# Optimization experiments

Hardware: AMD Instinct MI355X
Metric: run time of the kernel (lower is better)

The kernel has to match this reference:

```python
import jax, jax.numpy as jnp
import numpy as np

F = 39          # total fields = 13 numeric + 26 categorical
NUM_NUM = 13
N_CAT = 26
V = 100000      # vocab per categorical field
E = 16          # embed size
RED = max(1, F // 3)  # SE reduction size = 13
P = F * (F - 1) // 2  # 741 pairs
HID = [1024, 512, 256]
B = 4096

I_IDX, J_IDX = np.triu_indices(F, k=1)  # static pair indices, len P


def setup_inputs() -> dict:
    key = jax.random.key(0)
    ks = jax.random.split(key, 16)
    s = 0.01
    inp = {
        "cat": jax.random.randint(ks[0], (B, N_CAT), 0, V),
        "num": jax.random.normal(ks[1], (B, NUM_NUM), dtype=jnp.float32),
        "embed_tables": jax.random.normal(ks[2], (N_CAT, V, E), dtype=jnp.float32) * s,
        "num_emb": jax.random.normal(ks[3], (NUM_NUM, E), dtype=jnp.float32) * s,
        "W_se1": jax.random.normal(ks[4], (F, RED), dtype=jnp.float32) * 0.1,
        "W_se2": jax.random.normal(ks[5], (RED, F), dtype=jnp.float32) * 0.1,
        "W_bil": jax.random.normal(ks[6], (F, E, E), dtype=jnp.float32) * 0.1,  # per-field Linear(E,E,no bias), [field,in,out]
        "W_d1": jax.random.normal(ks[7], (2 * P * E, HID[0]), dtype=jnp.float32) * 0.01,
        "b_d1": jnp.zeros((HID[0],), dtype=jnp.float32),
        "W_d2": jax.random.normal(ks[8], (HID[0], HID[1]), dtype=jnp.float32) * 0.02,
        "b_d2": jnp.zeros((HID[1],), dtype=jnp.float32),
        "W_d3": jax.random.normal(ks[9], (HID[1], HID[2]), dtype=jnp.float32) * 0.02,
        "b_d3": jnp.zeros((HID[2],), dtype=jnp.float32),
        "W_out": jax.random.normal(ks[10], (HID[2], 1), dtype=jnp.float32) * 0.02,
        "b_out": jnp.zeros((1,), dtype=jnp.float32),
    }
    return inp


def _bilinear_each(x, W_bil):
    # x: [B,F,E]; project each field with its own matrix, then pairwise multiply.
    proj = jnp.einsum("bfe,fed->bfd", x, W_bil)            # [B,F,E]
    return proj[:, I_IDX, :] * x[:, J_IDX, :]               # [B,P,E]


def reference(cat, num, embed_tables, num_emb, W_se1, W_se2, W_bil,
              W_d1, b_d1, W_d2, b_d2, W_d3, b_d3, W_out, b_out):
    # categorical embeddings: per-field gather -> [B, N_CAT, E]
    cat_embed = embed_tables[jnp.arange(N_CAT)[None, :], cat]
    # numerical "embeddings": value * learned vector -> [B, NUM_NUM, E]
    num_embed = num[:, :, None] * num_emb[None, :, :]
    x = jnp.concatenate([num_embed, cat_embed], axis=1)     # [B,F,E]

    # SENET gating
    Z = jnp.mean(x, axis=-1)                                 # [B,F]
    A = jax.nn.relu(jax.nn.relu(Z @ W_se1) @ W_se2)          # [B,F]
    V = x * A[:, :, None]

    se_bi = _bilinear_each(V, W_bil)                         # [B,P,E]
    bi = _bilinear_each(x, W_bil)                            # [B,P,E]
    hid = jnp.concatenate([se_bi, bi], axis=1).reshape(x.shape[0], -1)  # [B, 2*P*E]

    h = jax.nn.relu(hid @ W_d1 + b_d1)
    h = jax.nn.relu(h @ W_d2 + b_d2)
    h = jax.nn.relu(h @ W_d3 + b_d3)
    return h @ W_out + b_out                                 # [B,1]
```

## Files before the change

### kernel.cpp

```cpp
#include <hip/hip_runtime.h>

typedef unsigned short u16;
typedef __attribute__((ext_vector_type(8))) __bf16 bf16x8;
typedef __attribute__((ext_vector_type(4))) float f32x4;
typedef __attribute__((ext_vector_type(4))) unsigned short u16x4;
typedef __attribute__((ext_vector_type(8))) unsigned short u16x8;

#define NF    39
#define NNUM  13
#define NCAT  26
#define VOC   100000
#define NPAIR 741
#define KHID  23712
#define BATCH 4096
#define HD1   1024
#define HD2   512
#define HD3   256

__device__ __forceinline__ u16 f2bf(float f) {
  unsigned u = __builtin_bit_cast(unsigned, f);
  return (u16)((u + 0x7fffu + ((u >> 16) & 1u)) >> 16);
}

__device__ __forceinline__ void gload16(const void* g, void* l) {
  __builtin_amdgcn_global_load_lds((const __attribute__((address_space(1))) void*)g,
                                   (__attribute__((address_space(3))) void*)l, 16, 0, 0);
}

__global__ __launch_bounds__(256) void fuse_front(
    const int* __restrict__ cat, const float* __restrict__ num,
    const float* __restrict__ tables, const float* __restrict__ nemb,
    const float* __restrict__ Wse1, const float* __restrict__ Wse2,
    const float* __restrict__ Wbil, u16* __restrict__ hid)
{
  __shared__ float xs[NF][16];
  __shared__ float wb[NF][16][16];
  __shared__ float pr[NF][16];
  __shared__ float Zs[NF], Ts[NNUM], As[NF];
  __shared__ unsigned char pis[NPAIR], pjs[NPAIR];

  const int b = blockIdx.x;
  const int tid = threadIdx.x;

  for (int i = tid; i < NF * 64; i += 256)
    ((f32x4*)wb)[i] = ((const f32x4*)Wbil)[i];

  for (int t = tid; t < NNUM * 16; t += 256) {
    int f = t >> 4, e = t & 15;
    xs[f][e] = num[b * NNUM + f] * nemb[t];
  }
  for (int t = tid; t < NCAT * 16; t += 256) {
    int c = t >> 4, e = t & 15;
    int cv = cat[b * NCAT + c];
    xs[NNUM + c][e] = tables[((size_t)c * VOC + cv) * 16 + e];
  }
  for (int p = tid; p < NPAIR; p += 256) {
    int i = 0, rs = 0;
    while (p >= rs + (NF - 1 - i)) { rs += NF - 1 - i; ++i; }
    pis[p] = (unsigned char)i;
    pjs[p] = (unsigned char)(i + 1 + (p - rs));
  }
  __syncthreads();

  if (tid < NF) {
    float s = 0.f;
    #pragma unroll
    for (int e = 0; e < 16; ++e) s += xs[tid][e];
    Zs[tid] = s * (1.f / 16.f);
  }
  __syncthreads();
  if (tid < NNUM) {
    float s = 0.f;
    for (int f = 0; f < NF; ++f) s += Zs[f] * Wse1[f * NNUM + tid];
    Ts[tid] = fmaxf(s, 0.f);
  }
  __syncthreads();
  if (tid < NF) {
    float s = 0.f;
    for (int r = 0; r < NNUM; ++r) s += Ts[r] * Wse2[r * NF + tid];
    As[tid] = fmaxf(s, 0.f);
  }
  for (int t = tid; t < NF * 16; t += 256) {
    int f = t >> 4, d = t & 15;
    float s = 0.f;
    #pragma unroll
    for (int e = 0; e < 16; ++e) s += xs[f][e] * wb[f][e][d];
    pr[f][d] = s;
  }
  __syncthreads();

  u16* hr = hid + (size_t)b * KHID;
  for (int idx2 = tid; idx2 < NPAIR * 2; idx2 += 256) {
    const int p = idx2 >> 1, e0 = (idx2 & 1) * 8;
    const int i = pis[p], j = pjs[p];
    const float aa = As[i] * As[j];
    u16x8 vb, vs;
    #pragma unroll
    for (int e = 0; e < 8; ++e) {
      float bv = pr[i][e0 + e] * xs[j][e0 + e];
      vb[e] = f2bf(bv);
      vs[e] = f2bf(aa * bv);
    }
    *reinterpret_cast<u16x8*>(hr + NPAIR * 16 + p * 16 + e0) = vb;
    *reinterpret_cast<u16x8*>(hr + p * 16 + e0) = vs;
  }
}

__global__ __launch_bounds__(256) void transpose_all(
    const float* __restrict__ Wd1, const float* __restrict__ Wd2,
    const float* __restrict__ Wd3, u16* __restrict__ W1t,
    u16* __restrict__ W2t, u16* __restrict__ W3t)
{
  __shared__ float t[32][33];
  const int bid = blockIdx.x;
  const float* in; u16* out; int K, N, kb, nb;
  if (bid < 741 * 32)        { in = Wd1; out = W1t; K = KHID; N = HD1; kb = bid % 741; nb = bid / 741; }
  else if (bid < 741 * 32 + 512) { int r = bid - 741 * 32; in = Wd2; out = W2t; K = HD1; N = HD2; kb = r % 32; nb = r / 32; }
  else                       { int r = bid - 741 * 32 - 512; in = Wd3; out = W3t; K = HD2; N = HD3; kb = r % 16; nb = r / 16; }

  const int k0 = kb * 32, n0 = nb * 32;
  const int c = threadIdx.x & 31, r = threadIdx.x >> 5;
  #pragma unroll
  for (int it = 0; it < 4; ++it)
    t[r + it * 8][c] = in[(size_t)(k0 + r + it * 8) * N + n0 + c];
  __syncthreads();
  const int n = threadIdx.x >> 3, kq = (threadIdx.x & 7) * 4;
  u16x4 v;
  #pragma unroll
  for (int q = 0; q < 4; ++q) v[q] = f2bf(t[kq + q][n]);
  *reinterpret_cast<u16x4*>(out + (size_t)(n0 + n) * K + k0 + kq) = v;
}

__global__ __launch_bounds__(512, 2) void gemm8p_bf16(
    const u16* __restrict__ A, const u16* __restrict__ Bt,
    float* __restrict__ Cp, int M, int N, int K, int totku, int kpb)
{
  __shared__ __align__(16) u16 lds[65536];

  const int tid = threadIdx.x;
  const int wid = tid >> 6, lane = tid & 63;

  const int d = blockIdx.x;
  const int x = d & 7, jj = d >> 3;
  const int mb = ((x & 3) << 2) | (jj & 3);
  const int nb = (jj >> 2) & 3;
  const int sb = ((x >> 2) << 1) | (jj >> 4);

  const int ks0 = sb * kpb;
  const int kunits = (totku - ks0 < kpb) ? (totku - ks0) : kpb;
  const int ftiles = kunits >> 1;

  const int wm = wid >> 2, wn = wid & 3;
  const int lrow = lane & 15, c0 = lane >> 4;

  const int rr = tid >> 2, cc = tid & 3, csrc = cc ^ ((rr >> 1) & 3);
  const u16* pAg = A  + (size_t)((size_t)mb * 256 + rr) * K + (size_t)ks0 * 32 + csrc * 8;
  const u16* pBg = Bt + (size_t)((size_t)nb * 256 + rr) * K + (size_t)ks0 * 32 + csrc * 8;
  const size_t rsk = (size_t)128 * K;
  const int dstoff = tid * 8;

  int offA[8], offB[4];
  #pragma unroll
  for (int m = 0; m < 8; ++m) {
    int r = wm * 128 + m * 16 + lrow;
    offA[m] = r * 32 + ((c0 ^ ((r >> 1) & 3)) << 3);
  }
  #pragma unroll
  for (int n = 0; n < 4; ++n) {
    int r = wn * 64 + n * 16 + lrow;
    offB[n] = r * 32 + ((c0 ^ ((r >> 1) & 3)) << 3);
  }

#define STAGE_A(g) { int sg = ((g) < kunits) ? (g) : (kunits - 1);          \
    const u16* s_ = pAg + (size_t)sg * 32;                                   \
    u16* dp_ = lds + (((g) & 3) * 8192) + dstoff;                            \
    gload16(s_, dp_); gload16(s_ + rsk, dp_ + 4096); }
#define STAGE_B(g) { int sg = ((g) < kunits) ? (g) : (kunits - 1);          \
    const u16* s_ = pBg + (size_t)sg * 32;                                   \
    u16* dp_ = lds + 32768 + (((g) & 3) * 8192) + dstoff;                    \
    gload16(s_, dp_); gload16(s_ + rsk, dp_ + 4096); }

  f32x4 acc[8][4];
  #pragma unroll
  for (int m = 0; m < 8; ++m)
    #pragma unroll
    for (int n = 0; n < 4; ++n) acc[m][n] = f32x4{0.f, 0.f, 0.f, 0.f};

  STAGE_A(0); STAGE_B(0); STAGE_A(1); STAGE_B(1); STAGE_A(2); STAGE_B(2); STAGE_B(3);
  asm volatile("s_waitcnt vmcnt(10)" ::: "memory");
  __builtin_amdgcn_s_barrier();

  bf16x8 a0, a1, a2, a3, bg0, bg1, bg2, bg3;

  for (int tt = 0; tt < ftiles; ++tt) {
    const int g0 = tt << 1;
    const u16* As0 = lds + ((g0 & 3) * 8192);
    const u16* As1 = lds + (((g0 + 1) & 3) * 8192);
    const u16* Bs0 = lds + 32768 + ((g0 & 3) * 8192);
    const u16* Bs1 = lds + 32768 + (((g0 + 1) & 3) * 8192);

    a0 = *reinterpret_cast<const bf16x8*>(As0 + offA[0]);
    a1 = *reinterpret_cast<const bf16x8*>(As0 + offA[1]);
    a2 = *reinterpret_cast<const bf16x8*>(As0 + offA[2]);
    a3 = *reinterpret_cast<const bf16x8*>(As0 + offA[3]);
    bg0 = *reinterpret_cast<const bf16x8*>(Bs0 + offB[0]);
    bg1 = *reinterpret_cast<const bf16x8*>(Bs0 + offB[1]);
    bg2 = *reinterpret_cast<const bf16x8*>(Bs0 + offB[2]);
    bg3 = *reinterpret_cast<const bf16x8*>(Bs0 + offB[3]);
    STAGE_A(g0 + 3);
    __builtin_amdgcn_sched_barrier(0);
    __builtin_amdgcn_s_barrier();
    asm volatile("s_waitcnt lgkmcnt(0)" ::: "memory");
    __builtin_amdgcn_sched_barrier(0);
    __builtin_amdgcn_s_setprio(1);
    acc[0][0] = __builtin_amdgcn_mfma_f32_16x16x32_bf16(a0, bg0, acc[0][0], 0, 0, 0);
    acc[0][1] = __builtin_amdgcn_mfma_f32_16x16x32_bf16(a0, bg1, acc[0][1], 0, 0, 0);
    acc[0][2] = __builtin_amdgcn_mfma_f32_16x16x32_bf16(a0, bg2, acc[0][2], 0, 0, 0);
    acc[0][3] = __builtin_amdgcn_mfma_f32_16x16x32_bf16(a0, bg3, acc[0][3], 0, 0, 0);
    acc[1][0] = __builtin_amdgcn_mfma_f32_16x16x32_bf16(a1, bg0, acc[1][0], 0, 0, 0);
    acc[1][1] = __builtin_amdgcn_mfma_f32_16x16x32_bf16(a1, bg1, acc[1][1], 0, 0, 0);
    acc[1][2] = __builtin_amdgcn_mfma_f32_16x16x32_bf16(a1, bg2, acc[1][2], 0, 0, 0);
    acc[1][3] = __builtin_amdgcn_mfma_f32_16x16x32_bf16(a1, bg3, acc[1][3], 0, 0, 0);
    acc[2][0] = __builtin_amdgcn_mfma_f32_16x16x32_bf16(a2, bg0, acc[2][0], 0, 0, 0);
    acc[2][1] = __builtin_amdgcn_mfma_f32_16x16x32_bf16(a2, bg1, acc[2][1], 0, 0, 0);
    acc[2][2] = __builtin_amdgcn_mfma_f32_16x16x32_bf16(a2, bg2, acc[2][2], 0, 0, 0);
    acc[2][3] = __builtin_amdgcn_mfma_f32_16x16x32_bf16(a2, bg3, acc[2][3], 0, 0, 0);
    acc[3][0] = __builtin_amdgcn_mfma_f32_16x16x32_bf16(a3, bg0, acc[3][0], 0, 0, 0);
    acc[3][1] = __builtin_amdgcn_mfma_f32_16x16x32_bf16(a3, bg1, acc[3][1], 0, 0, 0);
    acc[3][2] = __builtin_amdgcn_mfma_f32_16x16x32_bf16(a3, bg2, acc[3][2], 0, 0, 0);
    acc[3][3] = __builtin_amdgcn_mfma_f32_16x16x32_bf16(a3, bg3, acc[3][3], 0, 0, 0);
    __builtin_amdgcn_s_setprio(0);
    __builtin_amdgcn_sched_barrier(0);
    __builtin_amdgcn_s_barrier();

    a0 = *reinterpret_cast<const bf16x8*>(As0 + offA[4]);
    a1 = *reinterpret_cast<const bf16x8*>(As0 + offA[5]);
    a2 = *reinterpret_cast<const bf16x8*>(As0 + offA[6]);
    a3 = *reinterpret_cast<const bf16x8*>(As0 + offA[7]);
    STAGE_B(g0 + 4);
    __builtin_amdgcn_sched_barrier(0);
    __builtin_amdgcn_s_barrier();
    asm volatile("s_waitcnt lgkmcnt(0)" ::: "memory");
    __builtin_amdgcn_sched_barrier(0);
    __builtin_amdgcn_s_setprio(1);
    acc[4][0] = __builtin_amdgcn_mfma_f32_16x16x32_bf16(a0, bg0, acc[4][0], 0, 0, 0);
    acc[4][1] = __builtin_amdgcn_mfma_f32_16x16x32_bf16(a0, bg1, acc[4][1], 0, 0, 0);
    acc[4][2] = __builtin_amdgcn_mfma_f32_16x16x32_bf16(a0, bg2, acc[4][2], 0, 0, 0);
    acc[4][3] = __builtin_amdgcn_mfma_f32_16x16x32_bf16(a0, bg3, acc[4][3], 0, 0, 0);
    acc[5][0] = __builtin_amdgcn_mfma_f32_16x16x32_bf16(a1, bg0, acc[5][0], 0, 0, 0);
    acc[5][1] = __builtin_amdgcn_mfma_f32_16x16x32_bf16(a1, bg1, acc[5][1], 0, 0, 0);
    acc[5][2] = __builtin_amdgcn_mfma_f32_16x16x32_bf16(a1, bg2, acc[5][2], 0, 0, 0);
    acc[5][3] = __builtin_amdgcn_mfma_f32_16x16x32_bf16(a1, bg3, acc[5][3], 0, 0, 0);
    acc[6][0] = __builtin_amdgcn_mfma_f32_16x16x32_bf16(a2, bg0, acc[6][0], 0, 0, 0);
    acc[6][1] = __builtin_amdgcn_mfma_f32_16x16x32_bf16(a2, bg1, acc[6][1], 0, 0, 0);
    acc[6][2] = __builtin_amdgcn_mfma_f32_16x16x32_bf16(a2, bg2, acc[6][2], 0, 0, 0);
    acc[6][3] = __builtin_amdgcn_mfma_f32_16x16x32_bf16(a2, bg3, acc[6][3], 0, 0, 0);
    acc[7][0] = __builtin_amdgcn_mfma_f32_16x16x32_bf16(a3, bg0, acc[7][0], 0, 0, 0);
    acc[7][1] = __builtin_amdgcn_mfma_f32_16x16x32_bf16(a3, bg1, acc[7][1], 0, 0, 0);
    acc[7][2] = __builtin_amdgcn_mfma_f32_16x16x32_bf16(a3, bg2, acc[7][2], 0, 0, 0);
    acc[7][3] = __builtin_amdgcn_mfma_f32_16x16x32_bf16(a3, bg3, acc[7][3], 0, 0, 0);
    __builtin_amdgcn_s_setprio(0);
    __builtin_amdgcn_sched_barrier(0);
    asm volatile("s_waitcnt vmcnt(8)" ::: "memory");
    __builtin_amdgcn_s_barrier();

    a0 = *reinterpret_cast<const bf16x8*>(As1 + offA[0]);
    a1 = *reinterpret_cast<const bf16x8*>(As1 + offA[1]);
    a2 = *reinterpret_cast<const bf16x8*>(As1 + offA[2]);
    a3 = *reinterpret_cast<const bf16x8*>(As1 + offA[3]);
    bg0 = *reinterpret_cast<const bf16x8*>(Bs1 + offB[0]);
    bg1 = *reinterpret_cast<const bf16x8*>(Bs1 + offB[1]);
    bg2 = *reinterpret_cast<const bf16x8*>(Bs1 + offB[2]);
    bg3 = *reinterpret_cast<const bf16x8*>(Bs1 + offB[3]);
    STAGE_A(g0 + 4);
    __builtin_amdgcn_sched_barrier(0);
    __builtin_amdgcn_s_barrier();
    asm volatile("s_waitcnt lgkmcnt(0)" ::: "memory");
    __builtin_amdgcn_sched_barrier(0);
    __builtin_amdgcn_s_setprio(1);
    acc[0][0] = __builtin_amdgcn_mfma_f32_16x16x32_bf16(a0, bg0, acc[0][0], 0, 0, 0);
    acc[0][1] = __builtin_amdgcn_mfma_f32_16x16x32_bf16(a0, bg1, acc[0][1], 0, 0, 0);
    acc[0][2] = __builtin_amdgcn_mfma_f32_16x16x32_bf16(a0, bg2, acc[0][2], 0, 0, 0);
    acc[0][3] = __builtin_amdgcn_mfma_f32_16x16x32_bf16(a0, bg3, acc[0][3], 0, 0, 0);
    acc[1][0] = __builtin_amdgcn_mfma_f32_16x16x32_bf16(a1, bg0, acc[1][0], 0, 0, 0);
    acc[1][1] = __builtin_amdgcn_mfma_f32_16x16x32_bf16(a1, bg1, acc[1][1], 0, 0, 0);
    acc[1][2] = __builtin_amdgcn_mfma_f32_16x16x32_bf16(a1, bg2, acc[1][2], 0, 0, 0);
    acc[1][3] = __builtin_amdgcn_mfma_f32_16x16x32_bf16(a1, bg3, acc[1][3], 0, 0, 0);
    acc[2][0] = __builtin_amdgcn_mfma_f32_16x16x32_bf16(a2, bg0, acc[2][0], 0, 0, 0);
    acc[2][1] = __builtin_amdgcn_mfma_f32_16x16x32_bf16(a2, bg1, acc[2][1], 0, 0, 0);
    acc[2][2] = __builtin_amdgcn_mfma_f32_16x16x32_bf16(a2, bg2, acc[2][2], 0, 0, 0);
    acc[2][3] = __builtin_amdgcn_mfma_f32_16x16x32_bf16(a2, bg3, acc[2][3], 0, 0, 0);
    acc[3][0] = __builtin_amdgcn_mfma_f32_16x16x32_bf16(a3, bg0, acc[3][0], 0, 0, 0);
    acc[3][1] = __builtin_amdgcn_mfma_f32_16x16x32_bf16(a3, bg1, acc[3][1], 0, 0, 0);
    acc[3][2] = __builtin_amdgcn_mfma_f32_16x16x32_bf16(a3, bg2, acc[3][2], 0, 0, 0);
    acc[3][3] = __builtin_amdgcn_mfma_f32_16x16x32_bf16(a3, bg3, acc[3][3], 0, 0, 0);
    __builtin_amdgcn_s_setprio(0);
    __builtin_amdgcn_sched_barrier(0);
    __builtin_amdgcn_s_barrier();

    a0 = *reinterpret_cast<const bf16x8*>(As1 + offA[4]);
    a1 = *reinterpret_cast<const bf16x8*>(As1 + offA[5]);
    a2 = *reinterpret_cast<const bf16x8*>(As1 + offA[6]);
    a3 = *reinterpret_cast<const bf16x8*>(As1 + offA[7]);
    STAGE_B(g0 + 5);
    __builtin_amdgcn_sched_barrier(0);
    __builtin_amdgcn_s_barrier();
    asm volatile("s_waitcnt lgkmcnt(0)" ::: "memory");
    __builtin_amdgcn_sched_barrier(0);
    __builtin_amdgcn_s_setprio(1);
    acc[4][0] = __builtin_amdgcn_mfma_f32_16x16x32_bf16(a0, bg0, acc[4][0], 0, 0, 0);
    acc[4][1] = __builtin_amdgcn_mfma_f32_16x16x32_bf16(a0, bg1, acc[4][1], 0, 0, 0);
    acc[4][2] = __builtin_amdgcn_mfma_f32_16x16x32_bf16(a0, bg2, acc[4][2], 0, 0, 0);
    acc[4][3] = __builtin_amdgcn_mfma_f32_16x16x32_bf16(a0, bg3, acc[4][3], 0, 0, 0);
    acc[5][0] = __builtin_amdgcn_mfma_f32_16x16x32_bf16(a1, bg0, acc[5][0], 0, 0, 0);
    acc[5][1] = __builtin_amdgcn_mfma_f32_16x16x32_bf16(a1, bg1, acc[5][1], 0, 0, 0);
    acc[5][2] = __builtin_amdgcn_mfma_f32_16x16x32_bf16(a1, bg2, acc[5][2], 0, 0, 0);
    acc[5][3] = __builtin_amdgcn_mfma_f32_16x16x32_bf16(a1, bg3, acc[5][3], 0, 0, 0);
    acc[6][0] = __builtin_amdgcn_mfma_f32_16x16x32_bf16(a2, bg0, acc[6][0], 0, 0, 0);
    acc[6][1] = __builtin_amdgcn_mfma_f32_16x16x32_bf16(a2, bg1, acc[6][1], 0, 0, 0);
    acc[6][2] = __builtin_amdgcn_mfma_f32_16x16x32_bf16(a2, bg2, acc[6][2], 0, 0, 0);
    acc[6][3] = __builtin_amdgcn_mfma_f32_16x16x32_bf16(a2, bg3, acc[6][3], 0, 0, 0);
    acc[7][0] = __builtin_amdgcn_mfma_f32_16x16x32_bf16(a3, bg0, acc[7][0], 0, 0, 0);
    acc[7][1] = __builtin_amdgcn_mfma_f32_16x16x32_bf16(a3, bg1, acc[7][1], 0, 0, 0);
    acc[7][2] = __builtin_amdgcn_mfma_f32_16x16x32_bf16(a3, bg2, acc[7][2], 0, 0, 0);
    acc[7][3] = __builtin_amdgcn_mfma_f32_16x16x32_bf16(a3, bg3, acc[7][3], 0, 0, 0);
    __builtin_amdgcn_s_setprio(0);
    __builtin_amdgcn_sched_barrier(0);
    asm volatile("s_waitcnt vmcnt(8)" ::: "memory");
    __builtin_amdgcn_s_barrier();
  }

  if (kunits & 1) {
    asm volatile("s_waitcnt vmcnt(0)" ::: "memory");
    __builtin_amdgcn_s_barrier();
    const int g = kunits - 1;
    const u16* As = lds + ((g & 3) * 8192);
    const u16* Bs = lds + 32768 + ((g & 3) * 8192);
    bg0 = *reinterpret_cast<const bf16x8*>(Bs + offB[0]);
    bg1 = *reinterpret_cast<const bf16x8*>(Bs + offB[1]);
    bg2 = *reinterpret_cast<const bf16x8*>(Bs + offB[2]);
    bg3 = *reinterpret_cast<const bf16x8*>(Bs + offB[3]);
    #pragma unroll
    for (int m = 0; m < 8; ++m) {
      bf16x8 am = *reinterpret_cast<const bf16x8*>(As + offA[m]);
      acc[m][0] = __builtin_amdgcn_mfma_f32_16x16x32_bf16(am, bg0, acc[m][0], 0, 0, 0);
      acc[m][1] = __builtin_amdgcn_mfma_f32_16x16x32_bf16(am, bg1, acc[m][1], 0, 0, 0);
      acc[m][2] = __builtin_amdgcn_mfma_f32_16x16x32_bf16(am, bg2, acc[m][2], 0, 0, 0);
      acc[m][3] = __builtin_amdgcn_mfma_f32_16x16x32_bf16(am, bg3, acc[m][3], 0, 0, 0);
    }
  }
#undef STAGE_A
#undef STAGE_B

  float* C = Cp + (size_t)sb * M * N;
  #pragma unroll
  for (int m = 0; m < 8; ++m) {
    const int rb = mb * 256 + wm * 128 + m * 16 + (lane >> 4) * 4;
    #pragma unroll
    for (int n = 0; n < 4; ++n) {
      const int col = nb * 256 + wn * 64 + n * 16 + (lane & 15);
      #pragma unroll
      for (int j2 = 0; j2 < 4; ++j2)
        __builtin_nontemporal_store(acc[m][n][j2], &C[(size_t)(rb + j2) * N + col]);
    }
  }
}

__global__ __launch_bounds__(256) void gemm_bf16(
    const u16* __restrict__ A, const u16* __restrict__ Bt,
    float* __restrict__ Cp, int M, int N, int K, int kps)
{
  __shared__ __align__(16) u16 lA[128 * 32];
  __shared__ __align__(16) u16 lB[128 * 32];
  const int tid = threadIdx.x;
  const int mb = blockIdx.x, nb = blockIdx.y, sb = blockIdx.z;
  const int w = tid >> 6, lane = tid & 63;
  const int wr = (w >> 1) * 64, wc = (w & 1) * 64;
  const int lrow = lane & 15, lko = (lane >> 4) * 8;

  f32x4 acc[4][4];
  #pragma unroll
  for (int m = 0; m < 4; ++m)
    #pragma unroll
    for (int n = 0; n < 4; ++n) acc[m][n] = f32x4{0.f, 0.f, 0.f, 0.f};

  const u16* Ab = A + (size_t)mb * 128 * K;
  const u16* Bb = Bt + (size_t)nb * 128 * K;
  const int r0 = tid >> 2, inn = (tid & 3) * 8;
  const int l0 = (tid & ~63) * 8, l1 = ((256 + tid) & ~63) * 8;

  const int ks1 = (sb + 1) * kps;
  for (int ks = sb * kps; ks < ks1; ++ks) {
    const int k0 = ks * 32;
    __syncthreads();
    gload16(Ab + (size_t)r0 * K + k0 + inn,        lA + l0);
    gload16(Ab + (size_t)(r0 + 64) * K + k0 + inn, lA + l1);
    gload16(Bb + (size_t)r0 * K + k0 + inn,        lB + l0);
    gload16(Bb + (size_t)(r0 + 64) * K + k0 + inn, lB + l1);
    __syncthreads();
    bf16x8 af[4], bg[4];
    #pragma unroll
    for (int m = 0; m < 4; ++m)
      af[m] = *reinterpret_cast<const bf16x8*>(&lA[(wr + m * 16 + lrow) * 32 + lko]);
    #pragma unroll
    for (int n = 0; n < 4; ++n)
      bg[n] = *reinterpret_cast<const bf16x8*>(&lB[(wc + n * 16 + lrow) * 32 + lko]);
    #pragma unroll
    for (int m = 0; m < 4; ++m)
      #pragma unroll
      for (int n = 0; n < 4; ++n)
        acc[m][n] = __builtin_amdgcn_mfma_f32_16x16x32_bf16(af[m], bg[n], acc[m][n], 0, 0, 0);
  }

  float* C = Cp + (size_t)sb * M * N;
  #pragma unroll
  for (int m = 0; m < 4; ++m) {
    const int rb = mb * 128 + wr + m * 16 + (lane >> 4) * 4;
    #pragma unroll
    for (int n = 0; n < 4; ++n) {
      const int col = nb * 128 + wc + n * 16 + (lane & 15);
      #pragma unroll
      for (int j = 0; j < 4; ++j)
        __builtin_nontemporal_store(acc[m][n][j], &C[(size_t)(rb + j) * N + col]);
    }
  }
}

__global__ __launch_bounds__(256) void reduce_bias_relu_bf16(
    const float* __restrict__ part, int S, size_t MN,
    const float* __restrict__ bias, int nmask, u16* __restrict__ out)
{
  const size_t n8 = MN >> 3;
  for (size_t i8 = blockIdx.x * 256ull + threadIdx.x; i8 < n8; i8 += (size_t)gridDim.x * 256) {
    const size_t base = i8 * 8;
    f32x4 lo = {0.f, 0.f, 0.f, 0.f}, hi = {0.f, 0.f, 0.f, 0.f};
    for (int k = 0; k < S; ++k) {
      const float* p = part + (size_t)k * MN + base;
      f32x4 a = __builtin_nontemporal_load(reinterpret_cast<const f32x4*>(p));
      f32x4 b = __builtin_nontemporal_load(reinterpret_cast<const f32x4*>(p + 4));
      lo += a; hi += b;
    }
    const int bb = (int)(base & (size_t)nmask);
    const f32x4 b0 = *reinterpret_cast<const f32x4*>(bias + bb);
    const f32x4 b1 = *reinterpret_cast<const f32x4*>(bias + bb + 4);
    u16x8 v;
    #pragma unroll
    for (int e = 0; e < 4; ++e) v[e] = f2bf(fmaxf(lo[e] + b0[e], 0.f));
    #pragma unroll
    for (int e = 0; e < 4; ++e) v[4 + e] = f2bf(fmaxf(hi[e] + b1[e], 0.f));
    *reinterpret_cast<u16x8*>(out + base) = v;
  }
}

__global__ __launch_bounds__(256) void reduce_bias_relu_f32(
    const float* __restrict__ part, int S, size_t MN,
    const float* __restrict__ bias, int nmask, float* __restrict__ out)
{
  const size_t n8 = MN >> 3;
  for (size_t i8 = blockIdx.x * 256ull + threadIdx.x; i8 < n8; i8 += (size_t)gridDim.x * 256) {
    const size_t base = i8 * 8;
    f32x4 lo = {0.f, 0.f, 0.f, 0.f}, hi = {0.f, 0.f, 0.f, 0.f};
    for (int k = 0; k < S; ++k) {
      const float* p = part + (size_t)k * MN + base;
      f32x4 a = __builtin_nontemporal_load(reinterpret_cast<const f32x4*>(p));
      f32x4 b = __builtin_nontemporal_load(reinterpret_cast<const f32x4*>(p + 4));
      lo += a; hi += b;
    }
    const int bb = (int)(base & (size_t)nmask);
    const f32x4 b0 = *reinterpret_cast<const f32x4*>(bias + bb);
    const f32x4 b1 = *reinterpret_cast<const f32x4*>(bias + bb + 4);
    f32x4 o0, o1;
    #pragma unroll
    for (int e = 0; e < 4; ++e) { o0[e] = fmaxf(lo[e] + b0[e], 0.f); o1[e] = fmaxf(hi[e] + b1[e], 0.f); }
    *reinterpret_cast<f32x4*>(out + base) = o0;
    *reinterpret_cast<f32x4*>(out + base + 4) = o1;
  }
}

__global__ __launch_bounds__(256) void final_dot(
    const float* __restrict__ h3, const float* __restrict__ Wout,
    const float* __restrict__ bout, float* __restrict__ out)
{
  const int row = blockIdx.x * 4 + (threadIdx.x >> 6);
  const int lane = threadIdx.x & 63;
  const float* hr = h3 + (size_t)row * HD3;
  float s = 0.f;
  #pragma unroll
  for (int i = 0; i < 4; ++i) s += hr[lane + i * 64] * Wout[lane + i * 64];
  #pragma unroll
  for (int off = 32; off; off >>= 1) s += __shfl_down(s, off, 64);
  if (lane == 0) out[row] = s + bout[0];
}

extern "C" void kernel_launch(void* const* d_in, const int* in_sizes, int n_in,
                              void* d_out, int out_size, void* d_ws, size_t ws_size,
                              hipStream_t stream)
{
  const int*   cat    = (const int*)  d_in[0];
  const float* num    = (const float*)d_in[1];
  const float* tables = (const float*)d_in[2];
  const float* nemb   = (const float*)d_in[3];
  const float* Wse1   = (const float*)d_in[4];
  const float* Wse2   = (const float*)d_in[5];
  const float* Wbil   = (const float*)d_in[6];
  const float* Wd1    = (const float*)d_in[7];
  const float* bd1    = (const float*)d_in[8];
  const float* Wd2    = (const float*)d_in[9];
  const float* bd2    = (const float*)d_in[10];
  const float* Wd3    = (const float*)d_in[11];
  const float* bd3    = (const float*)d_in[12];
  const float* Wout   = (const float*)d_in[13];
  const float* bout   = (const float*)d_in[14];

  char* ws = (char*)d_ws;
  u16*   hid  = (u16*)  (ws + 0ull);
  u16*   W1t  = (u16*)  (ws + 194248704ull);
  float* part = (float*)(ws + 242810880ull);
  u16*   W2t  = (u16*)  (ws + 309919744ull);
  u16*   W3t  = (u16*)  (ws + 310968320ull);
  u16*   h1b  = (u16*)  (ws + 0ull);
  u16*   h2b  = (u16*)  (ws + 8388608ull);
  float* h3f  = (float*)(ws + 12582912ull);

  transpose_all<<<741 * 32 + 512 + 128, 256, 0, stream>>>(Wd1, Wd2, Wd3, W1t, W2t, W3t);
  fuse_front<<<BATCH, 256, 0, stream>>>(cat, num, tables, nemb, Wse1, Wse2, Wbil, hid);

  gemm8p_bf16<<<256, 512, 0, stream>>>(hid, W1t, part, BATCH, HD1, KHID, 741, 186);
  reduce_bias_relu_bf16<<<2048, 256, 0, stream>>>(part, 4, (size_t)BATCH * HD1, bd1, HD1 - 1, h1b);

  gemm_bf16<<<dim3(BATCH / 128, HD2 / 128, 2), 256, 0, stream>>>(h1b, W2t, part, BATCH, HD2, HD1, 16);
  reduce_bias_relu_bf16<<<1024, 256, 0, stream>>>(part, 2, (size_t)BATCH * HD2, bd2, HD2 - 1, h2b);

  gemm_bf16<<<dim3(BATCH / 128, HD3 / 128, 4), 256, 0, stream>>>(h2b, W3t, part, BATCH, HD3, HD2, 4);
  reduce_bias_relu_f32<<<512, 256, 0, stream>>>(part, 4, (size_t)BATCH * HD3, bd3, HD3 - 1, h3f);

  final_dot<<<BATCH / 4, 256, 0, stream>>>(h3f, Wout, bout, (float*)d_out);
}
```

Baseline: 343.2 us.

## Process two rows per front block, retune GEMM waits, fuse final reduce with dot

Each fuse_front block now handles two batch rows, which halves how often the bilinear weights are loaded into LDS and the pair tables are rebuilt. The last split-K reduction is fused with the output dot product, so the h3 buffer write/read and one launch are dropped. The gemm8p pipeline vmcnt waits are also changed: the prologue waits to 6, one mid-loop wait is removed and the end-of-loop wait is tightened to 6. The wait changes could make stages land later, or risk races if the counts are wrong.

```diff
diff --git a/kernel.cpp b/kernel.cpp
--- a/kernel.cpp
+++ b/kernel.cpp
@@ -33,26 +33,28 @@
     const float* __restrict__ Wse1, const float* __restrict__ Wse2,
     const float* __restrict__ Wbil, u16* __restrict__ hid)
 {
-  __shared__ float xs[NF][16];
+  __shared__ float xs[2][NF][16];
   __shared__ float wb[NF][16][16];
-  __shared__ float pr[NF][16];
-  __shared__ float Zs[NF], Ts[NNUM], As[NF];
+  __shared__ float pr[2][NF][16];
+  __shared__ float Zs[2][NF], Ts[2][NNUM], As[2][NF];
   __shared__ unsigned char pis[NPAIR], pjs[NPAIR];
 
-  const int b = blockIdx.x;
+  const int b0 = blockIdx.x * 2;
   const int tid = threadIdx.x;
 
   for (int i = tid; i < NF * 64; i += 256)
     ((f32x4*)wb)[i] = ((const f32x4*)Wbil)[i];
 
-  for (int t = tid; t < NNUM * 16; t += 256) {
-    int f = t >> 4, e = t & 15;
-    xs[f][e] = num[b * NNUM + f] * nemb[t];
-  }
-  for (int t = tid; t < NCAT * 16; t += 256) {
-    int c = t >> 4, e = t & 15;
-    int cv = cat[b * NCAT + c];
-    xs[NNUM + c][e] = tables[((size_t)c * VOC + cv) * 16 + e];
+  for (int t = tid; t < 2 * NNUM * 16; t += 256) {
+    int r = t / (NNUM * 16), t2 = t % (NNUM * 16);
+    int f = t2 >> 4, e = t2 & 15;
+    xs[r][f][e] = num[(b0 + r) * NNUM + f] * nemb[t2];
+  }
+  for (int t = tid; t < 2 * NCAT * 16; t += 256) {
+    int r = t / (NCAT * 16), t2 = t % (NCAT * 16);
+    int c = t2 >> 4, e = t2 & 15;
+    int cv = cat[(b0 + r) * NCAT + c];
+    xs[r][NNUM + c][e] = tables[((size_t)c * VOC + cv) * 16 + e];
   }
   for (int p = tid; p < NPAIR; p += 256) {
     int i = 0, rs = 0;
@@ -62,42 +64,47 @@
   }
   __syncthreads();
 
-  if (tid < NF) {
+  if (tid < 2 * NF) {
+    int r = tid / NF, f = tid % NF;
     float s = 0.f;
     #pragma unroll
-    for (int e = 0; e < 16; ++e) s += xs[tid][e];
-    Zs[tid] = s * (1.f / 16.f);
+    for (int e = 0; e < 16; ++e) s += xs[r][f][e];
+    Zs[r][f] = s * (1.f / 16.f);
   }
   __syncthreads();
-  if (tid < NNUM) {
+  if (tid < 2 * NNUM) {
+    int r = tid / NNUM, o = tid % NNUM;
     float s = 0.f;
-    for (int f = 0; f < NF; ++f) s += Zs[f] * Wse1[f * NNUM + tid];
-    Ts[tid] = fmaxf(s, 0.f);
+    for (int f = 0; f < NF; ++f) s += Zs[r][f] * Wse1[f * NNUM + o];
+    Ts[r][o] = fmaxf(s, 0.f);
   }
   __syncthreads();
-  if (tid < NF) {
+  if (tid < 2 * NF) {
+    int r = tid / NF, f = tid % NF;
     float s = 0.f;
-    for (int r = 0; r < NNUM; ++r) s += Ts[r] * Wse2[r * NF + tid];
-    As[tid] = fmaxf(s, 0.f);
-  }
-  for (int t = tid; t < NF * 16; t += 256) {
-    int f = t >> 4, d = t & 15;
+    for (int q = 0; q < NNUM; ++q) s += Ts[r][q] * Wse2[q * NF + f];
+    As[r][f] = fmaxf(s, 0.f);
+  }
+  for (int t = tid; t < 2 * NF * 16; t += 256) {
+    int r = t / (NF * 16), t2 = t % (NF * 16);
+    int f = t2 >> 4, d = t2 & 15;
     float s = 0.f;
     #pragma unroll
-    for (int e = 0; e < 16; ++e) s += xs[f][e] * wb[f][e][d];
-    pr[f][d] = s;
+    for (int e = 0; e < 16; ++e) s += xs[r][f][e] * wb[f][e][d];
+    pr[r][f][d] = s;
   }
   __syncthreads();
 
-  u16* hr = hid + (size_t)b * KHID;
-  for (int idx2 = tid; idx2 < NPAIR * 2; idx2 += 256) {
+  for (int idx = tid; idx < 2 * NPAIR * 2; idx += 256) {
+    const int r = idx / (NPAIR * 2), idx2 = idx % (NPAIR * 2);
     const int p = idx2 >> 1, e0 = (idx2 & 1) * 8;
     const int i = pis[p], j = pjs[p];
-    const float aa = As[i] * As[j];
+    const float aa = As[r][i] * As[r][j];
+    u16* hr = hid + (size_t)(b0 + r) * KHID;
     u16x8 vb, vs;
     #pragma unroll
     for (int e = 0; e < 8; ++e) {
-      float bv = pr[i][e0 + e] * xs[j][e0 + e];
+      float bv = pr[r][i][e0 + e] * xs[r][j][e0 + e];
       vb[e] = f2bf(bv);
       vs[e] = f2bf(aa * bv);
     }
@@ -187,7 +194,7 @@
     for (int n = 0; n < 4; ++n) acc[m][n] = f32x4{0.f, 0.f, 0.f, 0.f};
 
   STAGE_A(0); STAGE_B(0); STAGE_A(1); STAGE_B(1); STAGE_A(2); STAGE_B(2); STAGE_B(3);
-  asm volatile("s_waitcnt vmcnt(10)" ::: "memory");
+  asm volatile("s_waitcnt vmcnt(6)" ::: "memory");
   __builtin_amdgcn_s_barrier();
 
   bf16x8 a0, a1, a2, a3, bg0, bg1, bg2, bg3;
@@ -261,7 +268,6 @@
     acc[7][3] = __builtin_amdgcn_mfma_f32_16x16x32_bf16(a3, bg3, acc[7][3], 0, 0, 0);
     __builtin_amdgcn_s_setprio(0);
     __builtin_amdgcn_sched_barrier(0);
-    asm volatile("s_waitcnt vmcnt(8)" ::: "memory");
     __builtin_amdgcn_s_barrier();
 
     a0 = *reinterpret_cast<const bf16x8*>(As1 + offA[0]);
@@ -326,7 +332,7 @@
     acc[7][3] = __builtin_amdgcn_mfma_f32_16x16x32_bf16(a3, bg3, acc[7][3], 0, 0, 0);
     __builtin_amdgcn_s_setprio(0);
     __builtin_amdgcn_sched_barrier(0);
-    asm volatile("s_waitcnt vmcnt(8)" ::: "memory");
+    asm volatile("s_waitcnt vmcnt(6)" ::: "memory");
     __builtin_amdgcn_s_barrier();
   }
 
@@ -452,41 +458,26 @@
   }
 }
 
-__global__ __launch_bounds__(256) void reduce_bias_relu_f32(
-    const float* __restrict__ part, int S, size_t MN,
-    const float* __restrict__ bias, int nmask, float* __restrict__ out)
-{
-  const size_t n8 = MN >> 3;
-  for (size_t i8 = blockIdx.x * 256ull + threadIdx.x; i8 < n8; i8 += (size_t)gridDim.x * 256) {
-    const size_t base = i8 * 8;
-    f32x4 lo = {0.f, 0.f, 0.f, 0.f}, hi = {0.f, 0.f, 0.f, 0.f};
-    for (int k = 0; k < S; ++k) {
-      const float* p = part + (size_t)k * MN + base;
-      f32x4 a = __builtin_nontemporal_load(reinterpret_cast<const f32x4*>(p));
-      f32x4 b = __builtin_nontemporal_load(reinterpret_cast<const f32x4*>(p + 4));
-      lo += a; hi += b;
-    }
-    const int bb = (int)(base & (size_t)nmask);
-    const f32x4 b0 = *reinterpret_cast<const f32x4*>(bias + bb);
-    const f32x4 b1 = *reinterpret_cast<const f32x4*>(bias + bb + 4);
-    f32x4 o0, o1;
-    #pragma unroll
-    for (int e = 0; e < 4; ++e) { o0[e] = fmaxf(lo[e] + b0[e], 0.f); o1[e] = fmaxf(hi[e] + b1[e], 0.f); }
-    *reinterpret_cast<f32x4*>(out + base) = o0;
-    *reinterpret_cast<f32x4*>(out + base + 4) = o1;
-  }
-}
-
-__global__ __launch_bounds__(256) void final_dot(
-    const float* __restrict__ h3, const float* __restrict__ Wout,
-    const float* __restrict__ bout, float* __restrict__ out)
+__global__ __launch_bounds__(256) void reduce3_final(
+    const float* __restrict__ part, const float* __restrict__ bd3,
+    const float* __restrict__ Wout, const float* __restrict__ bout,
+    float* __restrict__ out)
 {
   const int row = blockIdx.x * 4 + (threadIdx.x >> 6);
   const int lane = threadIdx.x & 63;
-  const float* hr = h3 + (size_t)row * HD3;
+  const size_t MN = (size_t)BATCH * HD3;
+  const size_t base = (size_t)row * HD3;
   float s = 0.f;
   #pragma unroll
-  for (int i = 0; i < 4; ++i) s += hr[lane + i * 64] * Wout[lane + i * 64];
+  for (int i = 0; i < 4; ++i) {
+    const int e = lane + i * 64;
+    float v = 0.f;
+    #pragma unroll
+    for (int k = 0; k < 4; ++k)
+      v += __builtin_nontemporal_load(&part[(size_t)k * MN + base + e]);
+    v = fmaxf(v + bd3[e], 0.f);
+    s += v * Wout[e];
+  }
   #pragma unroll
   for (int off = 32; off; off >>= 1) s += __shfl_down(s, off, 64);
   if (lane == 0) out[row] = s + bout[0];
@@ -520,10 +511,9 @@
   u16*   W3t  = (u16*)  (ws + 310968320ull);
   u16*   h1b  = (u16*)  (ws + 0ull);
   u16*   h2b  = (u16*)  (ws + 8388608ull);
-  float* h3f  = (float*)(ws + 12582912ull);
 
   transpose_all<<<741 * 32 + 512 + 128, 256, 0, stream>>>(Wd1, Wd2, Wd3, W1t, W2t, W3t);
-  fuse_front<<<BATCH, 256, 0, stream>>>(cat, num, tables, nemb, Wse1, Wse2, Wbil, hid);
+  fuse_front<<<BATCH / 2, 256, 0, stream>>>(cat, num, tables, nemb, Wse1, Wse2, Wbil, hid);
 
   gemm8p_bf16<<<256, 512, 0, stream>>>(hid, W1t, part, BATCH, HD1, KHID, 741, 186);
   reduce_bias_relu_bf16<<<2048, 256, 0, stream>>>(part, 4, (size_t)BATCH * HD1, bd1, HD1 - 1, h1b);
@@ -532,7 +522,5 @@
   reduce_bias_relu_bf16<<<1024, 256, 0, stream>>>(part, 2, (size_t)BATCH * HD2, bd2, HD2 - 1, h2b);
 
   gemm_bf16<<<dim3(BATCH / 128, HD3 / 128, 4), 256, 0, stream>>>(h2b, W3t, part, BATCH, HD3, HD2, 4);
-  reduce_bias_relu_f32<<<512, 256, 0, stream>>>(part, 4, (size_t)BATCH * HD3, bd3, HD3 - 1, h3f);
-
-  final_dot<<<BATCH / 4, 256, 0, stream>>>(h3f, Wout, bout, (float*)d_out);
-}
+  reduce3_final<<<BATCH / 4, 256, 0, stream>>>(part, bd3, Wout, bout, (float*)d_out);
+}
```

Measured after the change: 332.4 us, median of 2. 1.03x faster.
